# Optimization experiments

Measured on AMD Instinct MI355X. Metric: run time of the kernel, lower is better.

The kernel has to match this reference:

```python
import jax, jax.numpy as jnp
import numpy as np
import math

DIM = 4096
BATCH = 8192
SCALE = 1.0 / math.sqrt(DIM)


def fwht(x):
    """Fast Walsh-Hadamard Transform along last axis (iterative butterfly).
    Faithful to the torch reshape/slice/cat implementation; the Python while
    loop is over log2(n) static stages, fine under jit.
    """
    n = x.shape[-1]
    h = 1
    while h < n:
        x = x.reshape(*x.shape[:-1], n // (2 * h), 2 * h)
        a = x[..., :h]
        b = x[..., h:]
        x = jnp.concatenate([a + b, a - b], axis=-1)
        x = x.reshape(*x.shape[:-2], n)
        h *= 2
    return x


def setup_inputs() -> dict:
    key = jax.random.key(0)
    kx, k1, k2, k3, k4 = jax.random.split(key, 5)
    x = jax.random.normal(kx, (BATCH, DIM), dtype=jnp.float32)
    # +/-1 random sign diagonals
    d1 = (jax.random.randint(k1, (DIM,), 0, 2).astype(jnp.float32) * 2 - 1)
    d2 = (jax.random.randint(k2, (DIM,), 0, 2).astype(jnp.float32) * 2 - 1)
    # |N(0,1)| gaussian diagonal
    gauss_d = jnp.abs(jax.random.normal(k3, (DIM,), dtype=jnp.float32))
    # random permutation of [0, DIM)
    perm = jax.random.permutation(k4, DIM).astype(jnp.int64)
    return {"x": x, "d1": d1, "d2": d2, "gauss_d": gauss_d, "perm": perm}


def reference(x, d1, d2, gauss_d, perm):
    # W ~= D2 @ H @ G @ Pi @ H @ D1, applied to each row of x
    y = x * d1
    y = fwht(y)
    y = y[..., perm]
    y = y * gauss_d
    y = fwht(y)
    y = y * d2
    return y * SCALE
```

## Files before the change

### kernel.cpp

```cpp
#include <hip/hip_runtime.h>

#define DIM 4096
#define FF_SCALE 0.015625f

__device__ __forceinline__ int phys(int i) {
    return i ^ ((((i >> 5) ^ (i >> 8) ^ (i >> 11)) & 7) << 2);
}

__device__ __forceinline__ void fwht16(float v[16]) {
#pragma unroll
    for (int h = 1; h < 16; h <<= 1) {
#pragma unroll
        for (int i = 0; i < 16; ++i) {
            if ((i & h) == 0) {
                float a = v[i], b = v[i + h];
                v[i] = a + b;
                v[i + h] = a - b;
            }
        }
    }
}

template <int CTRL>
__device__ __forceinline__ float qperm(float x) {
    return __int_as_float(
        __builtin_amdgcn_mov_dpp(__float_as_int(x), CTRL, 0xF, 0xF, true));
}

template <int CTRL>
__device__ __forceinline__ void qbutterfly(float v[16], float s) {
#pragma unroll
    for (int e = 0; e < 16; ++e) {
        float p = qperm<CTRL>(v[e]);
        v[e] = fmaf(v[e], s, p);
    }
}

__global__ __launch_bounds__(256) void fastfood_kernel(
    const float* __restrict__ x,
    const float* __restrict__ d1,
    const float* __restrict__ d2,
    const float* __restrict__ gauss_d,
    const int* __restrict__ perm,
    float* __restrict__ out)
{
    __shared__ float lds[DIM];
    const int t = threadIdx.x;
    const float s1 = (t & 1) ? -1.f : 1.f;
    const float s2 = (t & 2) ? -1.f : 1.f;
    const int B = (t >> 2) + ((t & 3) << 10);
    const size_t rowoff = (size_t)blockIdx.x * DIM;

    float v[16];

    {
        const float4* xv = (const float4*)(x + rowoff + t * 16);
        const float4* dv = (const float4*)(d1 + t * 16);
#pragma unroll
        for (int q = 0; q < 4; ++q) {
            float4 a = xv[q], d = dv[q];
            v[4 * q + 0] = a.x * d.x;
            v[4 * q + 1] = a.y * d.y;
            v[4 * q + 2] = a.z * d.z;
            v[4 * q + 3] = a.w * d.w;
        }
    }

    fwht16(v);
    qbutterfly<0xB1>(v, s1);
    qbutterfly<0x4E>(v, s2);

#pragma unroll
    for (int q = 0; q < 4; ++q)
        *(float4*)(lds + phys(t * 16 + 4 * q)) =
            make_float4(v[4 * q], v[4 * q + 1], v[4 * q + 2], v[4 * q + 3]);
    __syncthreads();

    float w[16];
#pragma unroll
    for (int c = 0; c < 16; ++c) w[c] = lds[phys(B + (c << 6))];
    fwht16(w);
    qbutterfly<0xB1>(w, s1);
    qbutterfly<0x4E>(w, s2);
#pragma unroll
    for (int c = 0; c < 16; ++c) lds[phys(B + (c << 6))] = w[c];
    __syncthreads();

    {
        const int4* pv = (const int4*)(perm + t * 16);
        const float4* gv = (const float4*)(gauss_d + t * 16);
#pragma unroll
        for (int q = 0; q < 4; ++q) {
            int4 p4 = pv[q];
            float4 g4 = gv[q];
            v[4 * q + 0] = lds[phys(p4.x)] * (g4.x * FF_SCALE);
            v[4 * q + 1] = lds[phys(p4.y)] * (g4.y * FF_SCALE);
            v[4 * q + 2] = lds[phys(p4.z)] * (g4.z * FF_SCALE);
            v[4 * q + 3] = lds[phys(p4.w)] * (g4.w * FF_SCALE);
        }
    }

    fwht16(v);
    qbutterfly<0xB1>(v, s1);
    qbutterfly<0x4E>(v, s2);
    __syncthreads();
#pragma unroll
    for (int q = 0; q < 4; ++q)
        *(float4*)(lds + phys(t * 16 + 4 * q)) =
            make_float4(v[4 * q], v[4 * q + 1], v[4 * q + 2], v[4 * q + 3]);
    __syncthreads();

#pragma unroll
    for (int c = 0; c < 16; ++c) w[c] = lds[phys(B + (c << 6))];
    fwht16(w);
    qbutterfly<0xB1>(w, s1);
    qbutterfly<0x4E>(w, s2);
#pragma unroll
    for (int c = 0; c < 16; ++c) {
        int i = B + (c << 6);
        out[rowoff + i] = w[c] * d2[i];
    }
}

extern "C" void kernel_launch(void* const* d_in, const int* in_sizes, int n_in,
                              void* d_out, int out_size, void* d_ws, size_t ws_size,
                              hipStream_t stream) {
    const float* x       = (const float*)d_in[0];
    const float* d1      = (const float*)d_in[1];
    const float* d2      = (const float*)d_in[2];
    const float* gauss_d = (const float*)d_in[3];
    const int*   perm    = (const int*)d_in[4];
    float* out = (float*)d_out;

    const int batch = in_sizes[0] / DIM;
    fastfood_kernel<<<batch, 256, 0, stream>>>(x, d1, d2, gauss_d, perm, out);
}
```

Before: 257.2 us.

## Process each row with a single 64-lane wavefront using 64-point register FWHTs

Replaces the 256-thread block, which combined 16-point register FWHTs with DPP quad butterflies, by a one-wavefront block where each lane holds 64 elements and does a full 64-point FWHT in registers. The two stages become a 64x64 transpose through a padded LDS slab (stride 68) instead of the XOR-swizzled layout. This removes the DPP cross-lane steps and keeps synchronisation inside a single wave. In exchange each thread needs far more registers, which may cut occupancy and latency hiding, and the wide per-lane float4 loads are poorly coalesced.

```diff
diff --git a/kernel.cpp b/kernel.cpp
--- a/kernel.cpp
+++ b/kernel.cpp
@@ -2,16 +2,15 @@
 
 #define DIM 4096
 #define FF_SCALE 0.015625f
+#define LDST 68
 
-__device__ __forceinline__ int phys(int i) {
-    return i ^ ((((i >> 5) ^ (i >> 8) ^ (i >> 11)) & 7) << 2);
-}
+__device__ __forceinline__ int pad(int i) { return i + ((i >> 6) << 2); }
 
-__device__ __forceinline__ void fwht16(float v[16]) {
+__device__ __forceinline__ void fwht64(float v[64]) {
 #pragma unroll
-    for (int h = 1; h < 16; h <<= 1) {
+    for (int h = 1; h < 64; h <<= 1) {
 #pragma unroll
-        for (int i = 0; i < 16; ++i) {
+        for (int i = 0; i < 64; ++i) {
             if ((i & h) == 0) {
                 float a = v[i], b = v[i + h];
                 v[i] = a + b;
@@ -21,22 +20,7 @@
     }
 }
 
-template <int CTRL>
-__device__ __forceinline__ float qperm(float x) {
-    return __int_as_float(
-        __builtin_amdgcn_mov_dpp(__float_as_int(x), CTRL, 0xF, 0xF, true));
-}
-
-template <int CTRL>
-__device__ __forceinline__ void qbutterfly(float v[16], float s) {
-#pragma unroll
-    for (int e = 0; e < 16; ++e) {
-        float p = qperm<CTRL>(v[e]);
-        v[e] = fmaf(v[e], s, p);
-    }
-}
-
-__global__ __launch_bounds__(256) void fastfood_kernel(
+__global__ __launch_bounds__(64) void fastfood_kernel(
     const float* __restrict__ x,
     const float* __restrict__ d1,
     const float* __restrict__ d2,
@@ -44,20 +28,17 @@
     const int* __restrict__ perm,
     float* __restrict__ out)
 {
-    __shared__ float lds[DIM];
-    const int t = threadIdx.x;
-    const float s1 = (t & 1) ? -1.f : 1.f;
-    const float s2 = (t & 2) ? -1.f : 1.f;
-    const int B = (t >> 2) + ((t & 3) << 10);
+    __shared__ float slab[64 * LDST];
+    const int l = threadIdx.x;
     const size_t rowoff = (size_t)blockIdx.x * DIM;
 
-    float v[16];
+    float v[64];
 
     {
-        const float4* xv = (const float4*)(x + rowoff + t * 16);
-        const float4* dv = (const float4*)(d1 + t * 16);
+        const float4* xv = (const float4*)(x + rowoff + l * 64);
+        const float4* dv = (const float4*)(d1 + l * 64);
 #pragma unroll
-        for (int q = 0; q < 4; ++q) {
+        for (int q = 0; q < 16; ++q) {
             float4 a = xv[q], d = dv[q];
             v[4 * q + 0] = a.x * d.x;
             v[4 * q + 1] = a.y * d.y;
@@ -66,59 +47,59 @@
         }
     }
 
-    fwht16(v);
-    qbutterfly<0xB1>(v, s1);
-    qbutterfly<0x4E>(v, s2);
+    fwht64(v);
+
+    {
+        float* wp = slab + l * LDST;
+#pragma unroll
+        for (int q = 0; q < 16; ++q)
+            *(float4*)(wp + 4 * q) =
+                make_float4(v[4 * q], v[4 * q + 1], v[4 * q + 2], v[4 * q + 3]);
+    }
+    __syncthreads();
 
 #pragma unroll
-    for (int q = 0; q < 4; ++q)
-        *(float4*)(lds + phys(t * 16 + 4 * q)) =
-            make_float4(v[4 * q], v[4 * q + 1], v[4 * q + 2], v[4 * q + 3]);
-    __syncthreads();
-
-    float w[16];
+    for (int c = 0; c < 64; ++c) v[c] = slab[l + LDST * c];
+    fwht64(v);
 #pragma unroll
-    for (int c = 0; c < 16; ++c) w[c] = lds[phys(B + (c << 6))];
-    fwht16(w);
-    qbutterfly<0xB1>(w, s1);
-    qbutterfly<0x4E>(w, s2);
-#pragma unroll
-    for (int c = 0; c < 16; ++c) lds[phys(B + (c << 6))] = w[c];
+    for (int c = 0; c < 64; ++c) slab[l + LDST * c] = v[c];
     __syncthreads();
 
     {
-        const int4* pv = (const int4*)(perm + t * 16);
-        const float4* gv = (const float4*)(gauss_d + t * 16);
+        const int4* pv = (const int4*)(perm + l * 64);
+        const float4* gv = (const float4*)(gauss_d + l * 64);
 #pragma unroll
-        for (int q = 0; q < 4; ++q) {
+        for (int q = 0; q < 16; ++q) {
             int4 p4 = pv[q];
             float4 g4 = gv[q];
-            v[4 * q + 0] = lds[phys(p4.x)] * (g4.x * FF_SCALE);
-            v[4 * q + 1] = lds[phys(p4.y)] * (g4.y * FF_SCALE);
-            v[4 * q + 2] = lds[phys(p4.z)] * (g4.z * FF_SCALE);
-            v[4 * q + 3] = lds[phys(p4.w)] * (g4.w * FF_SCALE);
+            v[4 * q + 0] = slab[pad(p4.x)] * (g4.x * FF_SCALE);
+            v[4 * q + 1] = slab[pad(p4.y)] * (g4.y * FF_SCALE);
+            v[4 * q + 2] = slab[pad(p4.z)] * (g4.z * FF_SCALE);
+            v[4 * q + 3] = slab[pad(p4.w)] * (g4.w * FF_SCALE);
         }
     }
 
-    fwht16(v);
-    qbutterfly<0xB1>(v, s1);
-    qbutterfly<0x4E>(v, s2);
+    fwht64(v);
     __syncthreads();
+
+    {
+        float* wp = slab + l * LDST;
 #pragma unroll
-    for (int q = 0; q < 4; ++q)
-        *(float4*)(lds + phys(t * 16 + 4 * q)) =
-            make_float4(v[4 * q], v[4 * q + 1], v[4 * q + 2], v[4 * q + 3]);
+        for (int q = 0; q < 16; ++q)
+            *(float4*)(wp + 4 * q) =
+                make_float4(v[4 * q], v[4 * q + 1], v[4 * q + 2], v[4 * q + 3]);
+    }
     __syncthreads();
 
 #pragma unroll
-    for (int c = 0; c < 16; ++c) w[c] = lds[phys(B + (c << 6))];
-    fwht16(w);
-    qbutterfly<0xB1>(w, s1);
-    qbutterfly<0x4E>(w, s2);
+    for (int c = 0; c < 64; ++c) v[c] = slab[l + LDST * c];
+    fwht64(v);
+    {
+        const float* d2p = d2 + l;
+        float* op = out + rowoff + l;
 #pragma unroll
-    for (int c = 0; c < 16; ++c) {
-        int i = B + (c << 6);
-        out[rowoff + i] = w[c] * d2[i];
+        for (int c = 0; c < 64; ++c)
+            op[64 * c] = v[c] * d2p[64 * c];
     }
 }
 
@@ -133,5 +114,5 @@
     float* out = (float*)d_out;
 
     const int batch = in_sizes[0] / DIM;
-    fastfood_kernel<<<batch, 256, 0, stream>>>(x, d1, d2, gauss_d, perm, out);
+    fastfood_kernel<<<batch, 64, 0, stream>>>(x, d1, d2, gauss_d, perm, out);
 }
```

Result: slower. 280.2 us (+9.0%).
